# Kernel tuning notes

Measured on AMD Instinct MI355X. Metric: run time of the kernel, lower is better.

The kernel has to match this reference:

```python
import jax, jax.numpy as jnp
import numpy as np

G = 56          # voxel grid resolution per axis
N = 65536
K = 27          # 3x3x3 kernel offsets
C_IN = 128
C_OUT = 128


def _build_rulebook():
    """Submanifold conv rulebook: for each kernel offset, (input_row, output_row) pairs.

    Padded to P=N pairs per offset; invalid pairs use in_idx=0 and out_idx=N
    (a dummy output slot that is dropped), so shapes are static.
    """
    rng = np.random.default_rng(0)
    keys = np.sort(rng.choice(G ** 3, size=N, replace=False)).astype(np.int64)
    x = keys // (G * G)
    y = (keys // G) % G
    z = keys % G
    in_idx = np.zeros((K, N), dtype=np.int32)
    out_idx = np.full((K, N), N, dtype=np.int32)
    k = 0
    for dx in (-1, 0, 1):
        for dy in (-1, 0, 1):
            for dz in (-1, 0, 1):
                nx, ny, nz = x + dx, y + dy, z + dz
                valid = (nx >= 0) & (nx < G) & (ny >= 0) & (ny < G) & (nz >= 0) & (nz < G)
                nkey = (nx * G + ny) * G + nz
                pos = np.searchsorted(keys, np.clip(nkey, 0, G ** 3 - 1))
                pos = np.clip(pos, 0, N - 1)
                found = valid & (keys[pos] == nkey)
                cnt = int(found.sum())
                in_idx[k, :cnt] = pos[found]
                out_idx[k, :cnt] = np.nonzero(found)[0]
                k += 1
    return jnp.asarray(in_idx), jnp.asarray(out_idx)


def setup_inputs() -> dict:
    key = jax.random.key(0)
    k1, k2, k3 = jax.random.split(key, 3)
    fan_in = K * C_IN
    features = jax.random.normal(k1, (N, C_IN), dtype=jnp.float32)
    weight = jax.random.normal(k2, (K, C_IN, C_OUT), dtype=jnp.float32) * (1.0 / np.sqrt(fan_in))
    bias = jax.random.normal(k3, (C_OUT,), dtype=jnp.float32) * 0.01
    in_idx, out_idx = _build_rulebook()
    return {"features": features, "weight": weight, "bias": bias,
            "in_idx": in_idx, "out_idx": out_idx}


def reference(features, weight, bias, in_idx, out_idx):
    # gather: [K, P, C_in]
    gathered = features[in_idx]
    # per-offset GEMM: [K, P, C_out]
    contrib = jnp.einsum('kpc,kcd->kpd', gathered, weight)
    n = features.shape[0]
    c_out = weight.shape[-1]
    # scatter-accumulate into N real rows + 1 dummy row for padded pairs
    out = jnp.zeros((n + 1, c_out), dtype=features.dtype)
    out = out.at[out_idx.reshape(-1)].add(contrib.reshape(-1, c_out))
    return out[:n] + bias
```

## Files before the change

### kernel.cpp

```cpp
#include <hip/hip_runtime.h>
#include <hip/hip_bf16.h>
#include <stdint.h>

#define NV   65536
#define KOFF 27
#define CIN  128
#define COUT 128
#define NSEC (NV + 128)

typedef __bf16 bf16x8 __attribute__((ext_vector_type(8)));
typedef float  f32x4  __attribute__((ext_vector_type(4)));

__device__ __forceinline__ void async_copy16(void* lds, const void* g) {
    __builtin_amdgcn_global_load_lds(
        (const __attribute__((address_space(1))) void*)g,
        (__attribute__((address_space(3))) void*)lds,
        16, 0, 0);
}

#define JOB_A_BLOCKS 4097
#define JOB_B_BLOCKS 216
#define JOB_S_BLOCKS 1728

__global__ void k_prep_all(const float* __restrict__ f,
                           uint4* __restrict__ fb4,
                           const float* __restrict__ w,
                           uint4* __restrict__ wfrag4,
                           const int4* __restrict__ in4,
                           const int4* __restrict__ out4,
                           int* __restrict__ nbr) {
    const int b = blockIdx.x;
    const int t = threadIdx.x;
    if (b < JOB_A_BLOCKS) {
        int i = b * 256 + t;
        int total8  = (NV + 1) * CIN / 8;
        int nvalid8 = NV * CIN / 8;
        if (i >= total8) return;
        union { uint4 u; __hip_bfloat16 h[8]; } p;
        if (i < nvalid8) {
            const float4* f4 = (const float4*)f;
            float4 a = f4[i * 2];
            float4 c = f4[i * 2 + 1];
            p.h[0] = __float2bfloat16(a.x);
            p.h[1] = __float2bfloat16(a.y);
            p.h[2] = __float2bfloat16(a.z);
            p.h[3] = __float2bfloat16(a.w);
            p.h[4] = __float2bfloat16(c.x);
            p.h[5] = __float2bfloat16(c.y);
            p.h[6] = __float2bfloat16(c.z);
            p.h[7] = __float2bfloat16(c.w);
        } else {
            p.u = make_uint4(0, 0, 0, 0);
        }
        fb4[i] = p.u;
    } else if (b < JOB_A_BLOCKS + JOB_B_BLOCKS) {
        int c    = (b - JOB_A_BLOCKS) * 256 + t;
        int lane = c & 63;
        int nt   = (c >> 6) & 1;
        int ks   = (c >> 7) & 3;
        int wv   = (c >> 9) & 3;
        int k    = c >> 11;
        int cout = wv * 32 + nt * 16 + (lane & 15);
        int cin0 = ks * 32 + (lane >> 4) * 8;
        const float* wk = w + k * 16384;
        union { uint4 u; __hip_bfloat16 h[8]; } p;
        #pragma unroll
        for (int j = 0; j < 8; ++j)
            p.h[j] = __float2bfloat16(wk[(cin0 + j) * 128 + cout]);
        wfrag4[c] = p.u;
    } else {
        int i = (b - JOB_A_BLOCKS - JOB_B_BLOCKS) * 256 + t;
        int k = i >> 14;
        int4 ii = in4[i];
        int4 oo = out4[i];
        int* nb = nbr + (size_t)k * NSEC;
        auto POS = [](int o) {
            return (o >> 7) * 128 + (o & 15) * 8 + ((o >> 4) & 7);
        };
        if ((unsigned)oo.x < NV) nb[POS(oo.x)] = ii.x;
        if ((unsigned)oo.y < NV) nb[POS(oo.y)] = ii.y;
        if ((unsigned)oo.z < NV) nb[POS(oo.z)] = ii.z;
        if ((unsigned)oo.w < NV) nb[POS(oo.w)] = ii.w;
    }
}

__global__ __launch_bounds__(256, 2)
void sp_conv_main(const __hip_bfloat16* __restrict__ feats,
                  const uint4* __restrict__ wfrag,
                  const int* __restrict__ nbrt,
                  const float* __restrict__ bias,
                  float* __restrict__ out) {
    __shared__ unsigned char smem[65536];

    const int t   = threadIdx.x;
    const int bid = blockIdx.x;
    const int tile0 = ((bid & 7) * 64 + (bid >> 3)) * 128;

    const int w    = t >> 6;
    const int lane = t & 63;
    const int lr   = lane & 15;
    const int quad = lane >> 4;

    const int srow  = t >> 4;
    const int sbyte = ((t & 15) ^ srow) * 16;

    f32x4 acc[8][2] = {};

    const unsigned char* featsB = (const unsigned char*)feats;

    int  arows[8];
    uint4 bA[4][2], bB[4][2];

    auto NLOAD = [&](int k) {
        const int4* np = (const int4*)(nbrt + (size_t)k * NSEC + tile0 + srow * 8);
        int4 a0 = np[0];
        int4 a1 = np[1];
        arows[0] = a0.x; arows[1] = a0.y; arows[2] = a0.z; arows[3] = a0.w;
        arows[4] = a1.x; arows[5] = a1.y; arows[6] = a1.z; arows[7] = a1.w;
    };
    auto STAGE = [&](int sb) {
        #pragma unroll
        for (int i = 0; i < 8; ++i) {
            unsigned ar = min((unsigned)arows[i], (unsigned)NV);
            async_copy16(smem + sb + i * 4096 + t * 16,
                         featsB + (size_t)ar * 256 + sbyte);
        }
    };
    auto BLOAD = [&](const uint4* wfk, uint4 (&b)[4][2]) {
        #pragma unroll
        for (int ks = 0; ks < 4; ++ks)
            #pragma unroll
            for (int nt = 0; nt < 2; ++nt)
                b[ks][nt] = wfk[ks * 128 + nt * 64];
    };
    auto AFLOAD = [&](int rb, int ks, bf16x8 (&af)[8]) {
        #pragma unroll
        for (int mt = 0; mt < 8; ++mt)
            af[mt] = *(const bf16x8*)(smem + rb + (mt * 16 + lr) * 256 +
                                      (((ks * 4 + quad) ^ lr) * 16));
    };
    auto MFMA16 = [&](bf16x8 (&af)[8], uint4 (&b)[2]) {
        #pragma unroll
        for (int mt = 0; mt < 8; ++mt)
            #pragma unroll
            for (int nt = 0; nt < 2; ++nt)
                acc[mt][nt] = __builtin_amdgcn_mfma_f32_16x16x32_bf16(
                    af[mt], *(const bf16x8*)&b[nt], acc[mt][nt], 0, 0, 0);
    };

    NLOAD(0);
    STAGE(0);
    __builtin_amdgcn_sched_barrier(0);
    NLOAD(1);
    BLOAD(wfrag + w * 512 + lane, bA);
    asm volatile("s_waitcnt vmcnt(10)" ::: "memory");
    __builtin_amdgcn_s_barrier();
    __builtin_amdgcn_sched_barrier(0);

    auto ITER = [&](int k, int rb, uint4 (&buse)[4][2], uint4 (&bload)[4][2]) {
        STAGE(rb ^ 32768);
        __builtin_amdgcn_sched_barrier(0);
        NLOAD(min(k + 2, KOFF - 1));
        BLOAD(wfrag + (k + 1) * 2048 + w * 512 + lane, bload);
        #pragma unroll
        for (int ks = 0; ks < 4; ++ks) {
            bf16x8 af[8];
            AFLOAD(rb, ks, af);
            __builtin_amdgcn_s_setprio(1);
            MFMA16(af, buse[ks]);
            __builtin_amdgcn_s_setprio(0);
        }
        __builtin_amdgcn_sched_barrier(0);
        asm volatile("s_waitcnt vmcnt(10)" ::: "memory");
        __builtin_amdgcn_s_barrier();
        __builtin_amdgcn_sched_barrier(0);
    };

    #pragma unroll 1
    for (int kk = 0; kk < KOFF - 1; kk += 2) {
        ITER(kk,     0,     bA, bB);
        ITER(kk + 1, 32768, bB, bA);
    }

    #pragma unroll
    for (int ks = 0; ks < 4; ++ks) {
        bf16x8 af[8];
        AFLOAD(0, ks, af);
        MFMA16(af, bA[ks]);
    }

    const int n0w = w * 32;
    float bv[2];
    #pragma unroll
    for (int nt = 0; nt < 2; ++nt) bv[nt] = bias[n0w + nt * 16 + lr];

    #pragma unroll
    for (int mt = 0; mt < 8; ++mt) {
        #pragma unroll
        for (int nt = 0; nt < 2; ++nt) {
            #pragma unroll
            for (int r = 0; r < 4; ++r) {
                int grow = tile0 + mt * 16 + quad * 4 + r;
                out[(size_t)grow * COUT + n0w + nt * 16 + lr] =
                    acc[mt][nt][r] + bv[nt];
            }
        }
    }
}


extern "C" void kernel_launch(void* const* d_in, const int* in_sizes, int n_in,
                              void* d_out, int out_size, void* d_ws, size_t ws_size,
                              hipStream_t stream) {
    const float* features = (const float*)d_in[0];
    const float* weight   = (const float*)d_in[1];
    const float* bias     = (const float*)d_in[2];
    const int*   in_idx   = (const int*)d_in[3];
    const int*   out_idx  = (const int*)d_in[4];
    float* out = (float*)d_out;

    uint8_t* ws = (uint8_t*)d_ws;
    size_t off = 0;
    __hip_bfloat16* feats_bf = (__hip_bfloat16*)(ws + off);
    off += (size_t)(NV + 1) * CIN * 2;
    off = (off + 255) & ~(size_t)255;
    uint4* wfrag = (uint4*)(ws + off);
    off += (size_t)KOFF * CIN * COUT * 2;
    off = (off + 255) & ~(size_t)255;
    int* nbr = (int*)(ws + off);

    hipMemsetAsync(nbr, 0xFF, (size_t)KOFF * NSEC * 4, stream);

    k_prep_all<<<JOB_A_BLOCKS + JOB_B_BLOCKS + JOB_S_BLOCKS, 256, 0, stream>>>(
        features, (uint4*)feats_bf, weight, wfrag,
        (const int4*)in_idx, (const int4*)out_idx, nbr);

    sp_conv_main<<<NV / 128, 256, 0, stream>>>(feats_bf, wfrag, nbr, bias, out);
}
```

Baseline: 149.7 us.

## Stage gathered features through registers with single LDS buffer for higher occupancy

Replaces the double-buffered async global-to-LDS staging (64KB) with a single 32KB LDS tile. The next offset's gathered rows are loaded into registers during compute and written to LDS after a barrier. Weight fragments are now reloaded per k-slice in place instead of double-buffered. Launch bounds are raised to 3 blocks per CU. The goal is more occupancy to hide gather latency, at the cost of an extra barrier per iteration, register-to-LDS stores, and register pressure that could cause spills. The vmcnt waits may also no longer match the new load counts.

```diff
diff --git a/kernel.cpp b/kernel.cpp
--- a/kernel.cpp
+++ b/kernel.cpp
@@ -84,13 +84,13 @@
     }
 }
 
-__global__ __launch_bounds__(256, 2)
+__global__ __launch_bounds__(256, 3)
 void sp_conv_main(const __hip_bfloat16* __restrict__ feats,
                   const uint4* __restrict__ wfrag,
                   const int* __restrict__ nbrt,
                   const float* __restrict__ bias,
                   float* __restrict__ out) {
-    __shared__ unsigned char smem[65536];
+    __shared__ unsigned char smem[32768];
 
     const int t   = threadIdx.x;
     const int bid = blockIdx.x;
@@ -105,11 +105,11 @@
     const int sbyte = ((t & 15) ^ srow) * 16;
 
     f32x4 acc[8][2] = {};
+    uint4 bcur[4][2];
+    uint4 sreg[8];
+    int   arows[8];
 
     const unsigned char* featsB = (const unsigned char*)feats;
-
-    int  arows[8];
-    uint4 bA[4][2], bB[4][2];
 
     auto NLOAD = [&](int k) {
         const int4* np = (const int4*)(nbrt + (size_t)k * NSEC + tile0 + srow * 8);
@@ -118,25 +118,17 @@
         arows[0] = a0.x; arows[1] = a0.y; arows[2] = a0.z; arows[3] = a0.w;
         arows[4] = a1.x; arows[5] = a1.y; arows[6] = a1.z; arows[7] = a1.w;
     };
-    auto STAGE = [&](int sb) {
+    auto SLOAD = [&]() {
         #pragma unroll
         for (int i = 0; i < 8; ++i) {
             unsigned ar = min((unsigned)arows[i], (unsigned)NV);
-            async_copy16(smem + sb + i * 4096 + t * 16,
-                         featsB + (size_t)ar * 256 + sbyte);
-        }
-    };
-    auto BLOAD = [&](const uint4* wfk, uint4 (&b)[4][2]) {
-        #pragma unroll
-        for (int ks = 0; ks < 4; ++ks)
-            #pragma unroll
-            for (int nt = 0; nt < 2; ++nt)
-                b[ks][nt] = wfk[ks * 128 + nt * 64];
-    };
-    auto AFLOAD = [&](int rb, int ks, bf16x8 (&af)[8]) {
+            sreg[i] = *(const uint4*)(featsB + (size_t)ar * 256 + sbyte);
+        }
+    };
+    auto AFLOAD = [&](int ks, bf16x8 (&af)[8]) {
         #pragma unroll
         for (int mt = 0; mt < 8; ++mt)
-            af[mt] = *(const bf16x8*)(smem + rb + (mt * 16 + lr) * 256 +
+            af[mt] = *(const bf16x8*)(smem + (mt * 16 + lr) * 256 +
                                       (((ks * 4 + quad) ^ lr) * 16));
     };
     auto MFMA16 = [&](bf16x8 (&af)[8], uint4 (&b)[2]) {
@@ -149,44 +141,60 @@
     };
 
     NLOAD(0);
-    STAGE(0);
+    #pragma unroll
+    for (int i = 0; i < 8; ++i) {
+        unsigned ar = min((unsigned)arows[i], (unsigned)NV);
+        async_copy16(smem + i * 4096 + t * 16,
+                     featsB + (size_t)ar * 256 + sbyte);
+    }
     __builtin_amdgcn_sched_barrier(0);
     NLOAD(1);
-    BLOAD(wfrag + w * 512 + lane, bA);
+    {
+        const uint4* wf0 = wfrag + w * 512 + lane;
+        #pragma unroll
+        for (int ks = 0; ks < 4; ++ks)
+            #pragma unroll
+            for (int nt = 0; nt < 2; ++nt)
+                bcur[ks][nt] = wf0[ks * 128 + nt * 64];
+    }
     asm volatile("s_waitcnt vmcnt(10)" ::: "memory");
     __builtin_amdgcn_s_barrier();
     __builtin_amdgcn_sched_barrier(0);
 
-    auto ITER = [&](int k, int rb, uint4 (&buse)[4][2], uint4 (&bload)[4][2]) {
-        STAGE(rb ^ 32768);
+    auto ITER = [&](int k) {
+        SLOAD();
         __builtin_amdgcn_sched_barrier(0);
         NLOAD(min(k + 2, KOFF - 1));
-        BLOAD(wfrag + (k + 1) * 2048 + w * 512 + lane, bload);
+        const uint4* wfn = wfrag + (k + 1) * 2048 + w * 512 + lane;
         #pragma unroll
         for (int ks = 0; ks < 4; ++ks) {
             bf16x8 af[8];
-            AFLOAD(rb, ks, af);
+            AFLOAD(ks, af);
             __builtin_amdgcn_s_setprio(1);
-            MFMA16(af, buse[ks]);
+            MFMA16(af, bcur[ks]);
             __builtin_amdgcn_s_setprio(0);
+            bcur[ks][0] = wfn[ks * 128];
+            bcur[ks][1] = wfn[ks * 128 + 64];
         }
         __builtin_amdgcn_sched_barrier(0);
         asm volatile("s_waitcnt vmcnt(10)" ::: "memory");
         __builtin_amdgcn_s_barrier();
+        #pragma unroll
+        for (int i = 0; i < 8; ++i)
+            *(uint4*)(smem + i * 4096 + t * 16) = sreg[i];
+        asm volatile("s_waitcnt lgkmcnt(0)" ::: "memory");
+        __builtin_amdgcn_s_barrier();
         __builtin_amdgcn_sched_barrier(0);
     };
 
     #pragma unroll 1
-    for (int kk = 0; kk < KOFF - 1; kk += 2) {
-        ITER(kk,     0,     bA, bB);
-        ITER(kk + 1, 32768, bB, bA);
-    }
+    for (int k = 0; k < KOFF - 1; ++k) ITER(k);
 
     #pragma unroll
     for (int ks = 0; ks < 4; ++ks) {
         bf16x8 af[8];
-        AFLOAD(0, ks, af);
-        MFMA16(af, bA[ks]);
+        AFLOAD(ks, af);
+        MFMA16(af, bcur[ks]);
     }
 
     const int n0w = w * 32;
```

After: 241.3 us. +61.2%, slower.

## Switch main GEMM to 32x32x16 bf16 MFMA with matching weight fragment layout

Applied to the files above, without the earlier changes.

Replaces the 16x16x32 MFMA tiling (8x2 tiles per wave) with 32x32x16 MFMA (4 tiles of 32 rows by the wave's 32 columns). The weight pre-swizzle, LDS A-fragment addressing, B fragment loads and output write indexing are all rewritten to match the new fragment layout. The larger instruction halves A-fragment LDS reads per MFMA and raises compute per instruction. In exchange the LDS reads may hit more bank conflicts under the existing XOR swizzle, and the output store pattern changes.

```diff
diff --git a/kernel.cpp b/kernel.cpp
--- a/kernel.cpp
+++ b/kernel.cpp
@@ -9,7 +9,7 @@
 #define NSEC (NV + 128)
 
 typedef __bf16 bf16x8 __attribute__((ext_vector_type(8)));
-typedef float  f32x4  __attribute__((ext_vector_type(4)));
+typedef float  f32x16 __attribute__((ext_vector_type(16)));
 
 __device__ __forceinline__ void async_copy16(void* lds, const void* g) {
     __builtin_amdgcn_global_load_lds(
@@ -56,12 +56,11 @@
     } else if (b < JOB_A_BLOCKS + JOB_B_BLOCKS) {
         int c    = (b - JOB_A_BLOCKS) * 256 + t;
         int lane = c & 63;
-        int nt   = (c >> 6) & 1;
-        int ks   = (c >> 7) & 3;
+        int ks   = (c >> 6) & 7;
         int wv   = (c >> 9) & 3;
         int k    = c >> 11;
-        int cout = wv * 32 + nt * 16 + (lane & 15);
-        int cin0 = ks * 32 + (lane >> 4) * 8;
+        int cout = wv * 32 + (lane & 31);
+        int cin0 = ks * 16 + (lane >> 5) * 8;
         const float* wk = w + k * 16384;
         union { uint4 u; __hip_bfloat16 h[8]; } p;
         #pragma unroll
@@ -99,17 +98,17 @@
     const int w    = t >> 6;
     const int lane = t & 63;
     const int lr   = lane & 15;
-    const int quad = lane >> 4;
+    const int l31  = lane & 31;
+    const int part = lane >> 5;
 
     const int srow  = t >> 4;
     const int sbyte = ((t & 15) ^ srow) * 16;
 
-    f32x4 acc[8][2] = {};
+    f32x16 acc[4] = {};
+    uint4 bA[8], bB[8];
+    int   arows[8];
 
     const unsigned char* featsB = (const unsigned char*)feats;
-
-    int  arows[8];
-    uint4 bA[4][2], bB[4][2];
 
     auto NLOAD = [&](int k) {
         const int4* np = (const int4*)(nbrt + (size_t)k * NSEC + tile0 + srow * 8);
@@ -126,26 +125,21 @@
                          featsB + (size_t)ar * 256 + sbyte);
         }
     };
-    auto BLOAD = [&](const uint4* wfk, uint4 (&b)[4][2]) {
-        #pragma unroll
-        for (int ks = 0; ks < 4; ++ks)
-            #pragma unroll
-            for (int nt = 0; nt < 2; ++nt)
-                b[ks][nt] = wfk[ks * 128 + nt * 64];
-    };
-    auto AFLOAD = [&](int rb, int ks, bf16x8 (&af)[8]) {
-        #pragma unroll
-        for (int mt = 0; mt < 8; ++mt)
-            af[mt] = *(const bf16x8*)(smem + rb + (mt * 16 + lr) * 256 +
-                                      (((ks * 4 + quad) ^ lr) * 16));
-    };
-    auto MFMA16 = [&](bf16x8 (&af)[8], uint4 (&b)[2]) {
-        #pragma unroll
-        for (int mt = 0; mt < 8; ++mt)
-            #pragma unroll
-            for (int nt = 0; nt < 2; ++nt)
-                acc[mt][nt] = __builtin_amdgcn_mfma_f32_16x16x32_bf16(
-                    af[mt], *(const bf16x8*)&b[nt], acc[mt][nt], 0, 0, 0);
+    auto BLOAD = [&](const uint4* wfk, uint4 (&b)[8]) {
+        #pragma unroll
+        for (int ks = 0; ks < 8; ++ks) b[ks] = wfk[ks * 64];
+    };
+    auto AFLOAD = [&](int rb, int ks, bf16x8 (&af)[4]) {
+        #pragma unroll
+        for (int mt = 0; mt < 4; ++mt)
+            af[mt] = *(const bf16x8*)(smem + rb + (mt * 32 + l31) * 256 +
+                                      (((ks * 2 + part) ^ lr) << 4));
+    };
+    auto MFMA4 = [&](bf16x8 (&af)[4], uint4& b) {
+        #pragma unroll
+        for (int mt = 0; mt < 4; ++mt)
+            acc[mt] = __builtin_amdgcn_mfma_f32_32x32x16_bf16(
+                af[mt], *(const bf16x8*)&b, acc[mt], 0, 0, 0);
     };
 
     NLOAD(0);
@@ -157,17 +151,17 @@
     __builtin_amdgcn_s_barrier();
     __builtin_amdgcn_sched_barrier(0);
 
-    auto ITER = [&](int k, int rb, uint4 (&buse)[4][2], uint4 (&bload)[4][2]) {
+    auto ITER = [&](int k, int rb, uint4 (&buse)[8], uint4 (&bload)[8]) {
         STAGE(rb ^ 32768);
         __builtin_amdgcn_sched_barrier(0);
         NLOAD(min(k + 2, KOFF - 1));
         BLOAD(wfrag + (k + 1) * 2048 + w * 512 + lane, bload);
         #pragma unroll
-        for (int ks = 0; ks < 4; ++ks) {
-            bf16x8 af[8];
+        for (int ks = 0; ks < 8; ++ks) {
+            bf16x8 af[4];
             AFLOAD(rb, ks, af);
             __builtin_amdgcn_s_setprio(1);
-            MFMA16(af, buse[ks]);
+            MFMA4(af, buse[ks]);
             __builtin_amdgcn_s_setprio(0);
         }
         __builtin_amdgcn_sched_barrier(0);
@@ -183,27 +177,20 @@
     }
 
     #pragma unroll
-    for (int ks = 0; ks < 4; ++ks) {
-        bf16x8 af[8];
+    for (int ks = 0; ks < 8; ++ks) {
+        bf16x8 af[4];
         AFLOAD(0, ks, af);
-        MFMA16(af, bA[ks]);
-    }
-
-    const int n0w = w * 32;
-    float bv[2];
+        MFMA4(af, bA[ks]);
+    }
+
+    const float bv = bias[w * 32 + l31];
+
     #pragma unroll
-    for (int nt = 0; nt < 2; ++nt) bv[nt] = bias[n0w + nt * 16 + lr];
-
-    #pragma unroll
-    for (int mt = 0; mt < 8; ++mt) {
-        #pragma unroll
-        for (int nt = 0; nt < 2; ++nt) {
-            #pragma unroll
-            for (int r = 0; r < 4; ++r) {
-                int grow = tile0 + mt * 16 + quad * 4 + r;
-                out[(size_t)grow * COUT + n0w + nt * 16 + lr] =
-                    acc[mt][nt][r] + bv[nt];
-            }
+    for (int mt = 0; mt < 4; ++mt) {
+        #pragma unroll
+        for (int r = 0; r < 16; ++r) {
+            int grow = tile0 + mt * 32 + (r & 3) + 8 * (r >> 2) + 4 * part;
+            out[(size_t)grow * COUT + w * 32 + l31] = acc[mt][r] + bv;
         }
     }
 }
```

New measurement: 157.5 us. 1.05x slower.
